# Kernel tuning notes

Hardware: AMD Instinct MI355X
Metric: run time of the kernel (lower is better)

Reference implementation:

```python
import jax, jax.numpy as jnp
import numpy as np

EMBED_DIM = 1024
NUM_HEADS = 16
HEAD_DIM = EMBED_DIM // NUM_HEADS


def setup_inputs() -> dict:
    key = jax.random.key(0)
    k1, k2, k3, k4, k5 = jax.random.split(key, 5)
    B, S, D = 2, 2048, EMBED_DIM
    s_in = 1.0 / np.sqrt(D)
    x = jax.random.normal(k1, (B, S, D), dtype=jnp.float32)
    W_qkv = jax.random.uniform(k2, (D, 3 * D), dtype=jnp.float32, minval=-s_in, maxval=s_in)
    b_qkv = jax.random.uniform(k3, (3 * D,), dtype=jnp.float32, minval=-s_in, maxval=s_in)
    W_out = jax.random.uniform(k4, (D, D), dtype=jnp.float32, minval=-s_in, maxval=s_in)
    b_out = jax.random.uniform(k5, (D,), dtype=jnp.float32, minval=-s_in, maxval=s_in)
    return {"x": x, "W_qkv": W_qkv, "b_qkv": b_qkv, "W_out": W_out, "b_out": b_out}


def reference(x, W_qkv, b_qkv, W_out, b_out):
    B, S, D = x.shape
    H, Hd = NUM_HEADS, HEAD_DIM
    qkv = x @ W_qkv + b_qkv                      # [B,S,3D]
    qkv = qkv.reshape(B, S, 3, H, Hd)
    q = qkv[:, :, 0].transpose(0, 2, 1, 3)       # [B,H,S,Hd]
    k = qkv[:, :, 1].transpose(0, 2, 1, 3)
    v = qkv[:, :, 2].transpose(0, 2, 1, 3)
    scores = jnp.einsum('bhsd,bhtd->bhst', q, k) / jnp.sqrt(jnp.float32(Hd))
    attn = jax.nn.softmax(scores, axis=-1)       # dropout is identity in eval mode
    out = jnp.einsum('bhst,bhtd->bhsd', attn, v)
    out = out.transpose(0, 2, 1, 3).reshape(B, S, D)
    return out @ W_out + b_out
```

## Files before the change

### kernel.cpp

```cpp
#include <hip/hip_runtime.h>
#include <stdint.h>
#include <math.h>

#define EMBED 1024
#define HEADS 16
#define HDIM  64
#define SEQ   2048
#define BATCH 2

typedef __bf16 bf16x8 __attribute__((ext_vector_type(8)));
typedef float  f32x4  __attribute__((ext_vector_type(4)));
typedef unsigned short u16x8 __attribute__((ext_vector_type(8)));
typedef unsigned short u16x4 __attribute__((ext_vector_type(4)));
typedef uint32_t u32x4v __attribute__((ext_vector_type(4)));

static __device__ __forceinline__ unsigned short f2bf(float f){
  union { float f; uint32_t u; } v; v.f = f;
  uint32_t u = v.u;
  uint32_t r = (u + 0x7FFFu + ((u >> 16) & 1u)) >> 16;
  return (unsigned short)r;
}
static __device__ __forceinline__ bf16x8 as_bf(u16x8 v){ return __builtin_bit_cast(bf16x8, v); }

static __device__ __forceinline__ uint32_t pk_bf16(float a, float b){
#if defined(__has_builtin) && __has_builtin(__builtin_amdgcn_cvt_pk_bf16_f32)
  typedef __bf16 bf16x2 __attribute__((ext_vector_type(2)));
  bf16x2 p = __builtin_amdgcn_cvt_pk_bf16_f32(a, b);
  return __builtin_bit_cast(uint32_t, p);
#else
  return (uint32_t)f2bf(a) | ((uint32_t)f2bf(b) << 16);
#endif
}

static __device__ __forceinline__ float fexp2(float x){
#if defined(__has_builtin) && __has_builtin(__builtin_amdgcn_exp2f)
  return __builtin_amdgcn_exp2f(x);
#else
  return exp2f(x);
#endif
}

static __device__ __forceinline__ void stage16(const unsigned short* gp,
                                               unsigned short* lp_wave, int lane){
#if defined(__has_builtin) && __has_builtin(__builtin_amdgcn_global_load_lds)
  __builtin_amdgcn_global_load_lds((const __attribute__((address_space(1))) void*)gp,
                                   (__attribute__((address_space(3))) void*)lp_wave,
                                   16, 0, 0);
#else
  *(u16x8*)(lp_wave + lane * 8) = *(const u16x8*)gp;
#endif
}

__global__ __launch_bounds__(256) void prep(
    const float* __restrict__ x,      unsigned short* __restrict__ xb,
    const float* __restrict__ W_qkv,  unsigned short* __restrict__ wqkvT,
    const float* __restrict__ W_out,  unsigned short* __restrict__ woutT)
{
  __shared__ unsigned short T[32 * 36];
  const int bid = blockIdx.x;
  const int t   = threadIdx.x;

  if (bid < 4096){
    int i = (bid * 256 + t) * 4;
    float4 v = *(const float4*)(x + i);
    u16x4 o;
    o[0] = f2bf(v.x); o[1] = f2bf(v.y); o[2] = f2bf(v.z); o[3] = f2bf(v.w);
    *(u16x4*)(xb + i) = o;
    return;
  }
  const float* W; unsigned short* Wt; int N, n0, k0;
  if (bid < 7168){
    int idx = bid - 4096;
    W = W_qkv; Wt = wqkvT; N = 3072;
    n0 = (idx % 96) * 32; k0 = (idx / 96) * 32;
  } else {
    int idx = bid - 7168;
    W = W_out; Wt = woutT; N = 1024;
    n0 = (idx & 31) * 32; k0 = (idx >> 5) * 32;
  }
  int kr = t >> 3, nc = (t & 7) * 4;
  float4 wv = *(const float4*)(W + (size_t)(k0 + kr) * N + n0 + nc);
  T[(nc + 0) * 36 + kr] = f2bf(wv.x);
  T[(nc + 1) * 36 + kr] = f2bf(wv.y);
  T[(nc + 2) * 36 + kr] = f2bf(wv.z);
  T[(nc + 3) * 36 + kr] = f2bf(wv.w);
  __syncthreads();
  int nr = t >> 3, kc = (t & 7) * 4;
  *(u16x4*)(Wt + (size_t)(n0 + nr) * 1024 + k0 + kc) = *(const u16x4*)&T[nr * 36 + kc];
}

__global__ __launch_bounds__(256) void vtrans(const unsigned short* __restrict__ V,
                                              unsigned short* __restrict__ VT){
  __shared__ unsigned short T[32 * 36];
  int t = threadIdx.x;
  int s0 = blockIdx.x * 32, d0 = blockIdx.y * 32;
  size_t base = (size_t)blockIdx.z * SEQ * HDIM;
  int sr = t >> 3, dc = (t & 7) * 4;
  u16x4 vv = *(const u16x4*)(V + base + (size_t)(s0 + sr) * HDIM + d0 + dc);
  T[(dc + 0) * 36 + sr] = vv[0];
  T[(dc + 1) * 36 + sr] = vv[1];
  T[(dc + 2) * 36 + sr] = vv[2];
  T[(dc + 3) * 36 + sr] = vv[3];
  __syncthreads();
  int dr = t >> 3, sc = (t & 7) * 4;
  int pos = (((sc >> 2) & 3) << 3) + (((sc >> 4) & 1) << 2);
  *(u16x4*)(VT + base + (size_t)(d0 + dr) * SEQ + s0 + pos) = *(const u16x4*)&T[dr * 36 + sc];
}

__global__ __launch_bounds__(256) void gemm_qkv(
    const unsigned short* __restrict__ A,
    const unsigned short* __restrict__ Bt,
    const float* __restrict__ bias,
    unsigned short* __restrict__ q_ws,
    unsigned short* __restrict__ k_ws,
    unsigned short* __restrict__ v_ws,
    int M, int N, int K)
{
  __shared__ unsigned short As[128 * 64];
  __shared__ unsigned short Bs[128 * 64];
  const int tid  = threadIdx.x;
  const int bm   = blockIdx.x, bn = blockIdx.y;
  const int w    = tid >> 6, lane = tid & 63;
  const int quad = lane >> 4, l16 = lane & 15;
  const int wm   = (w >> 1) * 64, wn = (w & 1) * 64;

  f32x4 acc[4][4] = {};

  for (int k0 = 0; k0 < K; k0 += 64) {
    #pragma unroll
    for (int i = 0; i < 4; i++){
      int c = w * 4 + i;
      int row = c * 8 + (lane >> 3);
      int kg = (lane & 7) ^ (row & 7);
      stage16(A  + (size_t)(bm * 128 + row) * K + k0 + kg * 8, &As[c * 512], lane);
      stage16(Bt + (size_t)(bn * 128 + row) * K + k0 + kg * 8, &Bs[c * 512], lane);
    }
    __syncthreads();

    #pragma unroll
    for (int kk = 0; kk < 2; kk++){
      bf16x8 af[4], bfr[4];
      #pragma unroll
      for (int t = 0; t < 4; t++){
        int ra = wm + t * 16 + l16;
        int rb = wn + t * 16 + l16;
        af[t]  = as_bf(*(const u16x8*)&As[(ra << 6) + ((((kk << 2) + quad) ^ (ra & 7)) << 3)]);
        bfr[t] = as_bf(*(const u16x8*)&Bs[(rb << 6) + ((((kk << 2) + quad) ^ (rb & 7)) << 3)]);
      }
      #pragma unroll
      for (int mt = 0; mt < 4; mt++)
        #pragma unroll
        for (int nt = 0; nt < 4; nt++)
          acc[mt][nt] = __builtin_amdgcn_mfma_f32_16x16x32_bf16(af[mt], bfr[nt], acc[mt][nt], 0, 0, 0);
    }
    __syncthreads();
  }

  const int which = (bn * 128) >> 10;
  unsigned short* dst = (which == 0) ? q_ws : (which == 1) ? k_ws : v_ws;
  const float scale = (which == 0) ? 0.18033688f : 1.0f;
  const int b = bm >> 4;
  #pragma unroll
  for (int nt = 0; nt < 4; nt++){
    int gnb = bn * 128 + wn + nt * 16;
    int h   = (gnb & 1023) >> 6;
    int hd  = (gnb & 63) + l16;
    float bv = bias[gnb + l16];
    unsigned short* dp = dst + (size_t)(b * HEADS + h) * SEQ * HDIM + hd;
    #pragma unroll
    for (int mt = 0; mt < 4; mt++){
      int s0 = ((bm & 15) * 128) + wm + mt * 16 + quad * 4;
      #pragma unroll
      for (int r = 0; r < 4; r++)
        dp[(size_t)(s0 + r) * HDIM] = f2bf((acc[mt][nt][r] + bv) * scale);
    }
  }
}

__global__ __launch_bounds__(256) void gemm_out(
    const unsigned short* __restrict__ A,
    const unsigned short* __restrict__ Bt,
    const float* __restrict__ bias,
    float* __restrict__ Cout,
    int M, int N, int K)
{
  __shared__ unsigned short As[128 * 64];
  __shared__ unsigned short Bs[64 * 64];
  const int tid  = threadIdx.x;
  const int bm   = blockIdx.x, bn = blockIdx.y;
  const int w    = tid >> 6, lane = tid & 63;
  const int quad = lane >> 4, l16 = lane & 15;
  const int wm   = (w >> 1) * 64, wn = (w & 1) * 32;

  f32x4 acc[4][2] = {};

  for (int k0 = 0; k0 < K; k0 += 64) {
    #pragma unroll
    for (int i = 0; i < 4; i++){
      int c = w * 4 + i;
      int row = c * 8 + (lane >> 3);
      int kg = (lane & 7) ^ (row & 7);
      stage16(A + (size_t)(bm * 128 + row) * K + k0 + kg * 8, &As[c * 512], lane);
    }
    #pragma unroll
    for (int i = 0; i < 2; i++){
      int c = w * 2 + i;
      int row = c * 8 + (lane >> 3);
      int kg = (lane & 7) ^ (row & 7);
      stage16(Bt + (size_t)(bn * 64 + row) * K + k0 + kg * 8, &Bs[c * 512], lane);
    }
    __syncthreads();

    #pragma unroll
    for (int kk = 0; kk < 2; kk++){
      bf16x8 af[4], bfr[2];
      #pragma unroll
      for (int t = 0; t < 4; t++){
        int ra = wm + t * 16 + l16;
        af[t] = as_bf(*(const u16x8*)&As[(ra << 6) + ((((kk << 2) + quad) ^ (ra & 7)) << 3)]);
      }
      #pragma unroll
      for (int t = 0; t < 2; t++){
        int rb = wn + t * 16 + l16;
        bfr[t] = as_bf(*(const u16x8*)&Bs[(rb << 6) + ((((kk << 2) + quad) ^ (rb & 7)) << 3)]);
      }
      #pragma unroll
      for (int mt = 0; mt < 4; mt++)
        #pragma unroll
        for (int nt = 0; nt < 2; nt++)
          acc[mt][nt] = __builtin_amdgcn_mfma_f32_16x16x32_bf16(af[mt], bfr[nt], acc[mt][nt], 0, 0, 0);
    }
    __syncthreads();
  }

  #pragma unroll
  for (int mt = 0; mt < 4; mt++)
    #pragma unroll
    for (int nt = 0; nt < 2; nt++)
      #pragma unroll
      for (int r = 0; r < 4; r++){
        int gm = bm * 128 + wm + mt * 16 + quad * 4 + r;
        int gn = bn * 64 + wn + nt * 16 + l16;
        Cout[(size_t)gm * N + gn] = acc[mt][nt][r] + bias[gn];
      }
}

__global__ __launch_bounds__(512) void attn(
    const unsigned short* __restrict__ q_ws,
    const unsigned short* __restrict__ k_ws,
    const unsigned short* __restrict__ vt_ws,
    unsigned short* __restrict__ o_ws)
{
  __shared__ unsigned short Qs[256 * 64];
  __shared__ unsigned short Ks[2][64 * 64];
  __shared__ unsigned short VTs[2][64 * 64];
  const int tid  = threadIdx.x;
  const int wgid = blockIdx.x;
  const int lin  = (wgid & 7) * 32 + (wgid >> 3);
  const int bh   = lin >> 3, qt = lin & 7;
  const int w    = tid >> 6, lane = tid & 63;
  const int quad = lane >> 4, l16 = lane & 15;
  const size_t base = (size_t)bh * SEQ * HDIM;

  #pragma unroll
  for (int i = 0; i < 4; i++){
    int c = w * 4 + i;
    int row = c * 8 + (lane >> 3);
    int kg = (lane & 7) ^ (row & 7);
    stage16(q_ws + base + (size_t)(qt * 256 + row) * HDIM + kg * 8, &Qs[c * 512], lane);
  }

  const int srow = w * 8 + (lane >> 3);
  const int skg  = (lane & 7) ^ (srow & 7);
  const int dofs = w * 512 + lane * 8;

  stage16(k_ws  + base + (size_t)srow * HDIM + skg * 8, &Ks[0][w * 512],  lane);
  stage16(vt_ws + base + (size_t)srow * SEQ + skg * 8,  &VTs[0][w * 512], lane);
  __syncthreads();

  bf16x8 bq[2][2];
  #pragma unroll
  for (int mq = 0; mq < 2; mq++){
    int row = w * 32 + mq * 16 + l16;
    #pragma unroll
    for (int ks = 0; ks < 2; ks++)
      bq[mq][ks] = as_bf(*(const u16x8*)&Qs[(row << 6) + ((((ks << 2) + quad) ^ (row & 7)) << 3)]);
  }

  const unsigned short* kp = k_ws  + base + (size_t)(64 + srow) * HDIM + skg * 8;
  const unsigned short* vp = vt_ws + base + (size_t)srow * SEQ + 64 + skg * 8;

  f32x4 acc[2][4] = {};
  float li[2] = {0.f, 0.f};

  for (int kt2 = 0; kt2 < SEQ / 128; kt2++){
    #pragma unroll
    for (int half = 0; half < 2; half++){
      const int cur = half;
      const int kt  = kt2 * 2 + half;
      u16x8 kpre, vpre;
      if (kt < SEQ / 64 - 1){
        kpre = *(const u16x8*)kp;  kp += 64 * HDIM;
        vpre = *(const u16x8*)vp;  vp += 64;
      }

      f32x4 sf[4][2] = {};
      #pragma unroll
      for (int ks = 0; ks < 2; ks++){
        #pragma unroll
        for (int nt = 0; nt < 4; nt++){
          int rk = nt * 16 + l16;
          bf16x8 ak = as_bf(*(const u16x8*)&Ks[cur][(rk << 6) + ((((ks << 2) + quad) ^ (rk & 7)) << 3)]);
          #pragma unroll
          for (int mq = 0; mq < 2; mq++)
            sf[nt][mq] = __builtin_amdgcn_mfma_f32_16x16x32_bf16(ak, bq[mq][ks], sf[nt][mq], 0, 0, 0);
        }
      }

      #pragma unroll
      for (int nt = 0; nt < 4; nt++)
        #pragma unroll
        for (int mq = 0; mq < 2; mq++)
          #pragma unroll
          for (int r = 0; r < 4; r++)
            sf[nt][mq][r] = fexp2(sf[nt][mq][r]);
      #pragma unroll
      for (int mq = 0; mq < 2; mq++)
        #pragma unroll
        for (int nt = 0; nt < 4; nt++)
          li[mq] += (sf[nt][mq][0] + sf[nt][mq][1]) + (sf[nt][mq][2] + sf[nt][mq][3]);

      #pragma unroll
      for (int c = 0; c < 2; c++){
        bf16x8 ap[2];
        #pragma unroll
        for (int mq = 0; mq < 2; mq++){
          u32x4v aw;
          aw[0] = pk_bf16(sf[c * 2][mq][0],     sf[c * 2][mq][1]);
          aw[1] = pk_bf16(sf[c * 2][mq][2],     sf[c * 2][mq][3]);
          aw[2] = pk_bf16(sf[c * 2 + 1][mq][0], sf[c * 2 + 1][mq][1]);
          aw[3] = pk_bf16(sf[c * 2 + 1][mq][2], sf[c * 2 + 1][mq][3]);
          ap[mq] = __builtin_bit_cast(bf16x8, aw);
        }
        #pragma unroll
        for (int nt = 0; nt < 4; nt++){
          int rv = nt * 16 + l16;
          bf16x8 bv = as_bf(*(const u16x8*)&VTs[cur][(rv << 6) + ((((c << 2) + quad) ^ (rv & 7)) << 3)]);
          #pragma unroll
          for (int mq = 0; mq < 2; mq++)
            acc[mq][nt] = __builtin_amdgcn_mfma_f32_16x16x32_bf16(ap[mq], bv, acc[mq][nt], 0, 0, 0);
        }
      }

      if (kt < SEQ / 64 - 1){
        *(u16x8*)&Ks[cur ^ 1][dofs]  = kpre;
        *(u16x8*)&VTs[cur ^ 1][dofs] = vpre;
      }
      __syncthreads();
    }
  }

  #pragma unroll
  for (int mq = 0; mq < 2; mq++){
    li[mq] += __shfl_xor(li[mq], 16);
    li[mq] += __shfl_xor(li[mq], 32);
  }
  float inv[2] = {1.0f / li[0], 1.0f / li[1]};
  float invr[2][4];
  #pragma unroll
  for (int mq = 0; mq < 2; mq++)
    #pragma unroll
    for (int r = 0; r < 4; r++)
      invr[mq][r] = __shfl(inv[mq], quad * 4 + r);

  int b = bh >> 4, h = bh & 15;
  #pragma unroll
  for (int mq = 0; mq < 2; mq++)
    #pragma unroll
    for (int nt = 0; nt < 4; nt++)
      #pragma unroll
      for (int r = 0; r < 4; r++){
        int s = qt * 256 + w * 32 + mq * 16 + quad * 4 + r;
        int d = h * 64 + nt * 16 + l16;
        o_ws[((size_t)(b * SEQ + s)) * EMBED + d] = f2bf(acc[mq][nt][r] * invr[mq][r]);
      }
}

extern "C" void kernel_launch(void* const* d_in, const int* in_sizes, int n_in,
                              void* d_out, int out_size, void* d_ws, size_t ws_size,
                              hipStream_t stream) {
  const float* x     = (const float*)d_in[0];
  const float* W_qkv = (const float*)d_in[1];
  const float* b_qkv = (const float*)d_in[2];
  const float* W_out = (const float*)d_in[3];
  const float* b_out = (const float*)d_in[4];
  float* out = (float*)d_out;

  char* ws = (char*)d_ws;
  unsigned short* xb    = (unsigned short*)(ws);
  unsigned short* vt    = (unsigned short*)(ws);
  unsigned short* q     = (unsigned short*)(ws + ((size_t)8  << 20));
  unsigned short* k     = (unsigned short*)(ws + ((size_t)16 << 20));
  unsigned short* v     = (unsigned short*)(ws + ((size_t)24 << 20));
  unsigned short* o     = (unsigned short*)(ws + ((size_t)24 << 20));
  unsigned short* wqkvT = (unsigned short*)(ws + ((size_t)32 << 20));
  unsigned short* woutT = (unsigned short*)(ws + ((size_t)38 << 20));

  prep<<<dim3(8192), dim3(256), 0, stream>>>(x, xb, W_qkv, wqkvT, W_out, woutT);

  gemm_qkv<<<dim3(32, 24), dim3(256), 0, stream>>>(
      xb, wqkvT, b_qkv, q, k, v, 4096, 3072, 1024);

  vtrans<<<dim3(64, 2, 32), dim3(256), 0, stream>>>(v, vt);

  attn<<<dim3(256), dim3(512), 0, stream>>>(q, k, vt, o);

  gemm_out<<<dim3(32, 16), dim3(256), 0, stream>>>(
      o, woutT, b_out, out, 4096, 1024, 1024);
}
```

Before: 197.5 us.

## Fuse V transpose into QKV GEMM epilogue and shrink attention blocks

```diff
diff --git a/kernel.cpp b/kernel.cpp
--- a/kernel.cpp
+++ b/kernel.cpp
@@ -89,31 +89,13 @@
   *(u16x4*)(Wt + (size_t)(n0 + nr) * 1024 + k0 + kc) = *(const u16x4*)&T[nr * 36 + kc];
 }
 
-__global__ __launch_bounds__(256) void vtrans(const unsigned short* __restrict__ V,
-                                              unsigned short* __restrict__ VT){
-  __shared__ unsigned short T[32 * 36];
-  int t = threadIdx.x;
-  int s0 = blockIdx.x * 32, d0 = blockIdx.y * 32;
-  size_t base = (size_t)blockIdx.z * SEQ * HDIM;
-  int sr = t >> 3, dc = (t & 7) * 4;
-  u16x4 vv = *(const u16x4*)(V + base + (size_t)(s0 + sr) * HDIM + d0 + dc);
-  T[(dc + 0) * 36 + sr] = vv[0];
-  T[(dc + 1) * 36 + sr] = vv[1];
-  T[(dc + 2) * 36 + sr] = vv[2];
-  T[(dc + 3) * 36 + sr] = vv[3];
-  __syncthreads();
-  int dr = t >> 3, sc = (t & 7) * 4;
-  int pos = (((sc >> 2) & 3) << 3) + (((sc >> 4) & 1) << 2);
-  *(u16x4*)(VT + base + (size_t)(d0 + dr) * SEQ + s0 + pos) = *(const u16x4*)&T[dr * 36 + sc];
-}
-
 __global__ __launch_bounds__(256) void gemm_qkv(
     const unsigned short* __restrict__ A,
     const unsigned short* __restrict__ Bt,
     const float* __restrict__ bias,
     unsigned short* __restrict__ q_ws,
     unsigned short* __restrict__ k_ws,
-    unsigned short* __restrict__ v_ws,
+    unsigned short* __restrict__ vt_ws,
     int M, int N, int K)
 {
   __shared__ unsigned short As[128 * 64];
@@ -157,9 +139,31 @@
   }
 
   const int which = (bn * 128) >> 10;
-  unsigned short* dst = (which == 0) ? q_ws : (which == 1) ? k_ws : v_ws;
+  const int b = bm >> 4;
+  const int S_base = (bm & 15) * 128 + wm;
+
+  if (which == 2){
+    #pragma unroll
+    for (int nt = 0; nt < 4; nt++){
+      int gnb = bn * 128 + wn + nt * 16;
+      int h   = (gnb & 1023) >> 6;
+      int d   = (gnb & 63) + l16;
+      float bv = bias[gnb + l16];
+      unsigned short* vp = vt_ws + (size_t)(b * HEADS + h) * SEQ * HDIM + (size_t)d * SEQ;
+      #pragma unroll
+      for (int mt = 0; mt < 4; mt++){
+        int spos = S_base + (mt >> 1) * 32 + quad * 8 + (mt & 1) * 4;
+        u16x4 o4;
+        #pragma unroll
+        for (int r = 0; r < 4; r++) o4[r] = f2bf(acc[mt][nt][r] + bv);
+        *(u16x4*)(vp + spos) = o4;
+      }
+    }
+    return;
+  }
+
+  unsigned short* dst = (which == 0) ? q_ws : k_ws;
   const float scale = (which == 0) ? 0.18033688f : 1.0f;
-  const int b = bm >> 4;
   #pragma unroll
   for (int nt = 0; nt < 4; nt++){
     int gnb = bn * 128 + wn + nt * 16;
@@ -169,7 +173,7 @@
     unsigned short* dp = dst + (size_t)(b * HEADS + h) * SEQ * HDIM + hd;
     #pragma unroll
     for (int mt = 0; mt < 4; mt++){
-      int s0 = ((bm & 15) * 128) + wm + mt * 16 + quad * 4;
+      int s0 = S_base + mt * 16 + quad * 4;
       #pragma unroll
       for (int r = 0; r < 4; r++)
         dp[(size_t)(s0 + r) * HDIM] = f2bf((acc[mt][nt][r] + bv) * scale);
@@ -245,145 +249,126 @@
       }
 }
 
-__global__ __launch_bounds__(512) void attn(
+__global__ __launch_bounds__(256, 4) void attn(
     const unsigned short* __restrict__ q_ws,
     const unsigned short* __restrict__ k_ws,
     const unsigned short* __restrict__ vt_ws,
     unsigned short* __restrict__ o_ws)
 {
-  __shared__ unsigned short Qs[256 * 64];
   __shared__ unsigned short Ks[2][64 * 64];
   __shared__ unsigned short VTs[2][64 * 64];
   const int tid  = threadIdx.x;
   const int wgid = blockIdx.x;
-  const int lin  = (wgid & 7) * 32 + (wgid >> 3);
-  const int bh   = lin >> 3, qt = lin & 7;
+  const int lin  = (wgid & 7) * 128 + (wgid >> 3);
+  const int bh   = lin >> 5, qt = lin & 31;
   const int w    = tid >> 6, lane = tid & 63;
   const int quad = lane >> 4, l16 = lane & 15;
   const size_t base = (size_t)bh * SEQ * HDIM;
 
-  #pragma unroll
-  for (int i = 0; i < 4; i++){
-    int c = w * 4 + i;
-    int row = c * 8 + (lane >> 3);
-    int kg = (lane & 7) ^ (row & 7);
-    stage16(q_ws + base + (size_t)(qt * 256 + row) * HDIM + kg * 8, &Qs[c * 512], lane);
-  }
-
-  const int srow = w * 8 + (lane >> 3);
-  const int skg  = (lane & 7) ^ (srow & 7);
-  const int dofs = w * 512 + lane * 8;
-
-  stage16(k_ws  + base + (size_t)srow * HDIM + skg * 8, &Ks[0][w * 512],  lane);
-  stage16(vt_ws + base + (size_t)srow * SEQ + skg * 8,  &VTs[0][w * 512], lane);
+  bf16x8 bq[2];
+  {
+    const int qrow = qt * 64 + w * 16 + l16;
+    #pragma unroll
+    for (int ks = 0; ks < 2; ks++)
+      bq[ks] = as_bf(*(const u16x8*)(q_ws + base + (size_t)qrow * HDIM + (ks * 4 + quad) * 8));
+  }
+
+  const int row0  = w * 16 + (lane >> 3);
+  const int row1  = row0 + 8;
+  const int kg0   = (lane & 7) ^ (row0 & 7);
+  const int kg1   = (lane & 7) ^ (row1 & 7);
+  const int dofs0 = (w * 2 + 0) * 512 + lane * 8;
+  const int dofs1 = (w * 2 + 1) * 512 + lane * 8;
+
+  stage16(k_ws  + base + (size_t)row0 * HDIM + kg0 * 8, &Ks[0][(w * 2 + 0) * 512], lane);
+  stage16(k_ws  + base + (size_t)row1 * HDIM + kg1 * 8, &Ks[0][(w * 2 + 1) * 512], lane);
+  stage16(vt_ws + base + (size_t)row0 * SEQ + kg0 * 8,  &VTs[0][(w * 2 + 0) * 512], lane);
+  stage16(vt_ws + base + (size_t)row1 * SEQ + kg1 * 8,  &VTs[0][(w * 2 + 1) * 512], lane);
   __syncthreads();
 
-  bf16x8 bq[2][2];
-  #pragma unroll
-  for (int mq = 0; mq < 2; mq++){
-    int row = w * 32 + mq * 16 + l16;
-    #pragma unroll
-    for (int ks = 0; ks < 2; ks++)
-      bq[mq][ks] = as_bf(*(const u16x8*)&Qs[(row << 6) + ((((ks << 2) + quad) ^ (row & 7)) << 3)]);
-  }
-
-  const unsigned short* kp = k_ws  + base + (size_t)(64 + srow) * HDIM + skg * 8;
-  const unsigned short* vp = vt_ws + base + (size_t)srow * SEQ + 64 + skg * 8;
-
-  f32x4 acc[2][4] = {};
-  float li[2] = {0.f, 0.f};
+  const unsigned short* kp0 = k_ws  + base + (size_t)(64 + row0) * HDIM + kg0 * 8;
+  const unsigned short* kp1 = k_ws  + base + (size_t)(64 + row1) * HDIM + kg1 * 8;
+  const unsigned short* vp0 = vt_ws + base + (size_t)row0 * SEQ + 64 + kg0 * 8;
+  const unsigned short* vp1 = vt_ws + base + (size_t)row1 * SEQ + 64 + kg1 * 8;
+
+  f32x4 acc[4] = {};
+  float li = 0.f;
 
   for (int kt2 = 0; kt2 < SEQ / 128; kt2++){
     #pragma unroll
     for (int half = 0; half < 2; half++){
       const int cur = half;
       const int kt  = kt2 * 2 + half;
-      u16x8 kpre, vpre;
+      u16x8 kpre0, kpre1, vpre0, vpre1;
       if (kt < SEQ / 64 - 1){
-        kpre = *(const u16x8*)kp;  kp += 64 * HDIM;
-        vpre = *(const u16x8*)vp;  vp += 64;
-      }
-
-      f32x4 sf[4][2] = {};
-      #pragma unroll
-      for (int ks = 0; ks < 2; ks++){
+        kpre0 = *(const u16x8*)kp0;  kp0 += 64 * HDIM;
+        kpre1 = *(const u16x8*)kp1;  kp1 += 64 * HDIM;
+        vpre0 = *(const u16x8*)vp0;  vp0 += 64;
+        vpre1 = *(const u16x8*)vp1;  vp1 += 64;
+      }
+
+      f32x4 sf[4] = {};
+      #pragma unroll
+      for (int ks = 0; ks < 2; ks++)
         #pragma unroll
         for (int nt = 0; nt < 4; nt++){
           int rk = nt * 16 + l16;
           bf16x8 ak = as_bf(*(const u16x8*)&Ks[cur][(rk << 6) + ((((ks << 2) + quad) ^ (rk & 7)) << 3)]);
-          #pragma unroll
-          for (int mq = 0; mq < 2; mq++)
-            sf[nt][mq] = __builtin_amdgcn_mfma_f32_16x16x32_bf16(ak, bq[mq][ks], sf[nt][mq], 0, 0, 0);
+          sf[nt] = __builtin_amdgcn_mfma_f32_16x16x32_bf16(ak, bq[ks], sf[nt], 0, 0, 0);
         }
-      }
 
       #pragma unroll
       for (int nt = 0; nt < 4; nt++)
         #pragma unroll
-        for (int mq = 0; mq < 2; mq++)
-          #pragma unroll
-          for (int r = 0; r < 4; r++)
-            sf[nt][mq][r] = fexp2(sf[nt][mq][r]);
-      #pragma unroll
-      for (int mq = 0; mq < 2; mq++)
-        #pragma unroll
-        for (int nt = 0; nt < 4; nt++)
-          li[mq] += (sf[nt][mq][0] + sf[nt][mq][1]) + (sf[nt][mq][2] + sf[nt][mq][3]);
+        for (int r = 0; r < 4; r++)
+          sf[nt][r] = fexp2(sf[nt][r]);
+      #pragma unroll
+      for (int nt = 0; nt < 4; nt++)
+        li += (sf[nt][0] + sf[nt][1]) + (sf[nt][2] + sf[nt][3]);
 
       #pragma unroll
       for (int c = 0; c < 2; c++){
-        bf16x8 ap[2];
-        #pragma unroll
-        for (int mq = 0; mq < 2; mq++){
-          u32x4v aw;
-          aw[0] = pk_bf16(sf[c * 2][mq][0],     sf[c * 2][mq][1]);
-          aw[1] = pk_bf16(sf[c * 2][mq][2],     sf[c * 2][mq][3]);
-          aw[2] = pk_bf16(sf[c * 2 + 1][mq][0], sf[c * 2 + 1][mq][1]);
-          aw[3] = pk_bf16(sf[c * 2 + 1][mq][2], sf[c * 2 + 1][mq][3]);
-          ap[mq] = __builtin_bit_cast(bf16x8, aw);
-        }
+        u32x4v aw;
+        aw[0] = pk_bf16(sf[c * 2][0],     sf[c * 2][1]);
+        aw[1] = pk_bf16(sf[c * 2][2],     sf[c * 2][3]);
+        aw[2] = pk_bf16(sf[c * 2 + 1][0], sf[c * 2 + 1][1]);
+        aw[3] = pk_bf16(sf[c * 2 + 1][2], sf[c * 2 + 1][3]);
+        bf16x8 ap = __builtin_bit_cast(bf16x8, aw);
         #pragma unroll
         for (int nt = 0; nt < 4; nt++){
           int rv = nt * 16 + l16;
           bf16x8 bv = as_bf(*(const u16x8*)&VTs[cur][(rv << 6) + ((((c << 2) + quad) ^ (rv & 7)) << 3)]);
-          #pragma unroll
-          for (int mq = 0; mq < 2; mq++)
-            acc[mq][nt] = __builtin_amdgcn_mfma_f32_16x16x32_bf16(ap[mq], bv, acc[mq][nt], 0, 0, 0);
+          acc[nt] = __builtin_amdgcn_mfma_f32_16x16x32_bf16(ap, bv, acc[nt], 0, 0, 0);
         }
       }
 
       if (kt < SEQ / 64 - 1){
-        *(u16x8*)&Ks[cur ^ 1][dofs]  = kpre;
-        *(u16x8*)&VTs[cur ^ 1][dofs] = vpre;
+        *(u16x8*)&Ks[cur ^ 1][dofs0]  = kpre0;
+        *(u16x8*)&Ks[cur ^ 1][dofs1]  = kpre1;
+        *(u16x8*)&VTs[cur ^ 1][dofs0] = vpre0;
+        *(u16x8*)&VTs[cur ^ 1][dofs1] = vpre1;
       }
       __syncthreads();
     }
   }
 
+  li += __shfl_xor(li, 16);
+  li += __shfl_xor(li, 32);
+  float inv = 1.0f / li;
+  float invr[4];
   #pragma unroll
-  for (int mq = 0; mq < 2; mq++){
-    li[mq] += __shfl_xor(li[mq], 16);
-    li[mq] += __shfl_xor(li[mq], 32);
-  }
-  float inv[2] = {1.0f / li[0], 1.0f / li[1]};
-  float invr[2][4];
-  #pragma unroll
-  for (int mq = 0; mq < 2; mq++)
-    #pragma unroll
-    for (int r = 0; r < 4; r++)
-      invr[mq][r] = __shfl(inv[mq], quad * 4 + r);
+  for (int r = 0; r < 4; r++)
+    invr[r] = __shfl(inv, quad * 4 + r);
 
   int b = bh >> 4, h = bh & 15;
   #pragma unroll
-  for (int mq = 0; mq < 2; mq++)
-    #pragma unroll
-    for (int nt = 0; nt < 4; nt++)
-      #pragma unroll
-      for (int r = 0; r < 4; r++){
-        int s = qt * 256 + w * 32 + mq * 16 + quad * 4 + r;
-        int d = h * 64 + nt * 16 + l16;
-        o_ws[((size_t)(b * SEQ + s)) * EMBED + d] = f2bf(acc[mq][nt][r] * invr[mq][r]);
-      }
+  for (int nt = 0; nt < 4; nt++)
+    #pragma unroll
+    for (int r = 0; r < 4; r++){
+      int s = qt * 64 + w * 16 + quad * 4 + r;
+      int d = h * 64 + nt * 16 + l16;
+      o_ws[((size_t)(b * SEQ + s)) * EMBED + d] = f2bf(acc[nt][r] * invr[r]);
+    }
 }
 
 extern "C" void kernel_launch(void* const* d_in, const int* in_sizes, int n_in,
@@ -398,22 +383,19 @@
 
   char* ws = (char*)d_ws;
   unsigned short* xb    = (unsigned short*)(ws);
-  unsigned short* vt    = (unsigned short*)(ws);
+  unsigned short* o     = (unsigned short*)(ws);
   unsigned short* q     = (unsigned short*)(ws + ((size_t)8  << 20));
   unsigned short* k     = (unsigned short*)(ws + ((size_t)16 << 20));
-  unsigned short* v     = (unsigned short*)(ws + ((size_t)24 << 20));
-  unsigned short* o     = (unsigned short*)(ws + ((size_t)24 << 20));
+  unsigned short* vt    = (unsigned short*)(ws + ((size_t)24 << 20));
   unsigned short* wqkvT = (unsigned short*)(ws + ((size_t)32 << 20));
   unsigned short* woutT = (unsigned short*)(ws + ((size_t)38 << 20));
 
   prep<<<dim3(8192), dim3(256), 0, stream>>>(x, xb, W_qkv, wqkvT, W_out, woutT);
 
   gemm_qkv<<<dim3(32, 24), dim3(256), 0, stream>>>(
-      xb, wqkvT, b_qkv, q, k, v, 4096, 3072, 1024);
-
-  vtrans<<<dim3(64, 2, 32), dim3(256), 0, stream>>>(v, vt);
-
-  attn<<<dim3(256), dim3(512), 0, stream>>>(q, k, vt, o);
+      xb, wqkvT, b_qkv, q, k, vt, 4096, 3072, 1024);
+
+  attn<<<dim3(1024), dim3(256), 0, stream>>>(q, k, vt, o);
 
   gemm_out<<<dim3(32, 16), dim3(256), 0, stream>>>(
       o, woutT, b_out, out, 4096, 1024, 1024);
```

Result: faster. 191.9 us (-2.8%).

## Split pipeline by batch and co-schedule attention with GEMMs in combo kernels

Applied to the files above, without the earlier changes.

```diff
diff --git a/kernel.cpp b/kernel.cpp
--- a/kernel.cpp
+++ b/kernel.cpp
@@ -89,37 +89,19 @@
   *(u16x4*)(Wt + (size_t)(n0 + nr) * 1024 + k0 + kc) = *(const u16x4*)&T[nr * 36 + kc];
 }
 
-__global__ __launch_bounds__(256) void vtrans(const unsigned short* __restrict__ V,
-                                              unsigned short* __restrict__ VT){
-  __shared__ unsigned short T[32 * 36];
-  int t = threadIdx.x;
-  int s0 = blockIdx.x * 32, d0 = blockIdx.y * 32;
-  size_t base = (size_t)blockIdx.z * SEQ * HDIM;
-  int sr = t >> 3, dc = (t & 7) * 4;
-  u16x4 vv = *(const u16x4*)(V + base + (size_t)(s0 + sr) * HDIM + d0 + dc);
-  T[(dc + 0) * 36 + sr] = vv[0];
-  T[(dc + 1) * 36 + sr] = vv[1];
-  T[(dc + 2) * 36 + sr] = vv[2];
-  T[(dc + 3) * 36 + sr] = vv[3];
-  __syncthreads();
-  int dr = t >> 3, sc = (t & 7) * 4;
-  int pos = (((sc >> 2) & 3) << 3) + (((sc >> 4) & 1) << 2);
-  *(u16x4*)(VT + base + (size_t)(d0 + dr) * SEQ + s0 + pos) = *(const u16x4*)&T[dr * 36 + sc];
-}
-
-__global__ __launch_bounds__(256) void gemm_qkv(
+static __device__ __forceinline__ void gemm_qkv_body(
+    int bm, int bn, unsigned short* SM,
     const unsigned short* __restrict__ A,
     const unsigned short* __restrict__ Bt,
     const float* __restrict__ bias,
     unsigned short* __restrict__ q_ws,
     unsigned short* __restrict__ k_ws,
-    unsigned short* __restrict__ v_ws,
-    int M, int N, int K)
-{
-  __shared__ unsigned short As[128 * 64];
-  __shared__ unsigned short Bs[128 * 64];
+    unsigned short* __restrict__ vt_ws)
+{
+  unsigned short* As = SM;
+  unsigned short* Bs = SM + 8192;
+  const int K = 1024;
   const int tid  = threadIdx.x;
-  const int bm   = blockIdx.x, bn = blockIdx.y;
   const int w    = tid >> 6, lane = tid & 63;
   const int quad = lane >> 4, l16 = lane & 15;
   const int wm   = (w >> 1) * 64, wn = (w & 1) * 64;
@@ -132,8 +114,8 @@
       int c = w * 4 + i;
       int row = c * 8 + (lane >> 3);
       int kg = (lane & 7) ^ (row & 7);
-      stage16(A  + (size_t)(bm * 128 + row) * K + k0 + kg * 8, &As[c * 512], lane);
-      stage16(Bt + (size_t)(bn * 128 + row) * K + k0 + kg * 8, &Bs[c * 512], lane);
+      stage16(A  + (size_t)(bm * 128 + row) * K + k0 + kg * 8, As + c * 512, lane);
+      stage16(Bt + (size_t)(bn * 128 + row) * K + k0 + kg * 8, Bs + c * 512, lane);
     }
     __syncthreads();
 
@@ -157,9 +139,31 @@
   }
 
   const int which = (bn * 128) >> 10;
-  unsigned short* dst = (which == 0) ? q_ws : (which == 1) ? k_ws : v_ws;
+  const int b = bm >> 4;
+  const int S_base = (bm & 15) * 128 + wm;
+
+  if (which == 2){
+    #pragma unroll
+    for (int nt = 0; nt < 4; nt++){
+      int gnb = bn * 128 + wn + nt * 16;
+      int h   = (gnb & 1023) >> 6;
+      int d   = (gnb & 63) + l16;
+      float bv = bias[gnb + l16];
+      unsigned short* vp = vt_ws + (size_t)(b * HEADS + h) * SEQ * HDIM + (size_t)d * SEQ;
+      #pragma unroll
+      for (int mt = 0; mt < 4; mt++){
+        int spos = S_base + (mt >> 1) * 32 + quad * 8 + (mt & 1) * 4;
+        u16x4 o4;
+        #pragma unroll
+        for (int r = 0; r < 4; r++) o4[r] = f2bf(acc[mt][nt][r] + bv);
+        *(u16x4*)(vp + spos) = o4;
+      }
+    }
+    return;
+  }
+
+  unsigned short* dst = (which == 0) ? q_ws : k_ws;
   const float scale = (which == 0) ? 0.18033688f : 1.0f;
-  const int b = bm >> 4;
   #pragma unroll
   for (int nt = 0; nt < 4; nt++){
     int gnb = bn * 128 + wn + nt * 16;
@@ -169,7 +173,7 @@
     unsigned short* dp = dst + (size_t)(b * HEADS + h) * SEQ * HDIM + hd;
     #pragma unroll
     for (int mt = 0; mt < 4; mt++){
-      int s0 = ((bm & 15) * 128) + wm + mt * 16 + quad * 4;
+      int s0 = S_base + mt * 16 + quad * 4;
       #pragma unroll
       for (int r = 0; r < 4; r++)
         dp[(size_t)(s0 + r) * HDIM] = f2bf((acc[mt][nt][r] + bv) * scale);
@@ -177,17 +181,17 @@
   }
 }
 
-__global__ __launch_bounds__(256) void gemm_out(
+static __device__ __forceinline__ void gemm_out_body(
+    int bm, int bn, unsigned short* SM,
     const unsigned short* __restrict__ A,
     const unsigned short* __restrict__ Bt,
     const float* __restrict__ bias,
-    float* __restrict__ Cout,
-    int M, int N, int K)
-{
-  __shared__ unsigned short As[128 * 64];
-  __shared__ unsigned short Bs[64 * 64];
+    float* __restrict__ Cout)
+{
+  unsigned short* As = SM;
+  unsigned short* Bs = SM + 8192;
+  const int K = 1024, N = 1024;
   const int tid  = threadIdx.x;
-  const int bm   = blockIdx.x, bn = blockIdx.y;
   const int w    = tid >> 6, lane = tid & 63;
   const int quad = lane >> 4, l16 = lane & 15;
   const int wm   = (w >> 1) * 64, wn = (w & 1) * 32;
@@ -200,14 +204,14 @@
       int c = w * 4 + i;
       int row = c * 8 + (lane >> 3);
       int kg = (lane & 7) ^ (row & 7);
-      stage16(A + (size_t)(bm * 128 + row) * K + k0 + kg * 8, &As[c * 512], lane);
+      stage16(A + (size_t)(bm * 128 + row) * K + k0 + kg * 8, As + c * 512, lane);
     }
     #pragma unroll
     for (int i = 0; i < 2; i++){
       int c = w * 2 + i;
       int row = c * 8 + (lane >> 3);
       int kg = (lane & 7) ^ (row & 7);
-      stage16(Bt + (size_t)(bn * 64 + row) * K + k0 + kg * 8, &Bs[c * 512], lane);
+      stage16(Bt + (size_t)(bn * 64 + row) * K + k0 + kg * 8, Bs + c * 512, lane);
     }
     __syncthreads();
 
@@ -245,119 +249,114 @@
       }
 }
 
-__global__ __launch_bounds__(512) void attn(
+static __device__ __forceinline__ void attn_body(
+    int abid, int bh_base, unsigned short* SM,
     const unsigned short* __restrict__ q_ws,
     const unsigned short* __restrict__ k_ws,
     const unsigned short* __restrict__ vt_ws,
     unsigned short* __restrict__ o_ws)
 {
-  __shared__ unsigned short Qs[256 * 64];
-  __shared__ unsigned short Ks[2][64 * 64];
-  __shared__ unsigned short VTs[2][64 * 64];
+  unsigned short* Ks  = SM;
+  unsigned short* VTs = SM + 8192;
   const int tid  = threadIdx.x;
-  const int wgid = blockIdx.x;
-  const int lin  = (wgid & 7) * 32 + (wgid >> 3);
-  const int bh   = lin >> 3, qt = lin & 7;
+  const int bh   = bh_base + (abid >> 4);
+  const int qt   = abid & 15;
   const int w    = tid >> 6, lane = tid & 63;
   const int quad = lane >> 4, l16 = lane & 15;
   const size_t base = (size_t)bh * SEQ * HDIM;
 
-  #pragma unroll
-  for (int i = 0; i < 4; i++){
-    int c = w * 4 + i;
-    int row = c * 8 + (lane >> 3);
-    int kg = (lane & 7) ^ (row & 7);
-    stage16(q_ws + base + (size_t)(qt * 256 + row) * HDIM + kg * 8, &Qs[c * 512], lane);
-  }
-
-  const int srow = w * 8 + (lane >> 3);
-  const int skg  = (lane & 7) ^ (srow & 7);
-  const int dofs = w * 512 + lane * 8;
-
-  stage16(k_ws  + base + (size_t)srow * HDIM + skg * 8, &Ks[0][w * 512],  lane);
-  stage16(vt_ws + base + (size_t)srow * SEQ + skg * 8,  &VTs[0][w * 512], lane);
+  bf16x8 bq[2][2];
+  #pragma unroll
+  for (int mq = 0; mq < 2; mq++){
+    int qrow = qt * 128 + w * 32 + mq * 16 + l16;
+    #pragma unroll
+    for (int ks = 0; ks < 2; ks++)
+      bq[mq][ks] = as_bf(*(const u16x8*)(q_ws + base + (size_t)qrow * HDIM + (ks * 4 + quad) * 8));
+  }
+
+  const int row0 = w * 16 + (lane >> 3), row1 = row0 + 8;
+  const int kg0 = (lane & 7) ^ (row0 & 7), kg1 = (lane & 7) ^ (row1 & 7);
+  const int dofs0 = (w * 2) * 512 + lane * 8, dofs1 = dofs0 + 512;
+
+  stage16(k_ws  + base + (size_t)row0 * HDIM + kg0 * 8, Ks  + (w * 2) * 512,     lane);
+  stage16(k_ws  + base + (size_t)row1 * HDIM + kg1 * 8, Ks  + (w * 2 + 1) * 512, lane);
+  stage16(vt_ws + base + (size_t)row0 * SEQ + kg0 * 8,  VTs + (w * 2) * 512,     lane);
+  stage16(vt_ws + base + (size_t)row1 * SEQ + kg1 * 8,  VTs + (w * 2 + 1) * 512, lane);
   __syncthreads();
 
-  bf16x8 bq[2][2];
-  #pragma unroll
-  for (int mq = 0; mq < 2; mq++){
-    int row = w * 32 + mq * 16 + l16;
-    #pragma unroll
-    for (int ks = 0; ks < 2; ks++)
-      bq[mq][ks] = as_bf(*(const u16x8*)&Qs[(row << 6) + ((((ks << 2) + quad) ^ (row & 7)) << 3)]);
-  }
-
-  const unsigned short* kp = k_ws  + base + (size_t)(64 + srow) * HDIM + skg * 8;
-  const unsigned short* vp = vt_ws + base + (size_t)srow * SEQ + 64 + skg * 8;
+  const unsigned short* kp0 = k_ws  + base + (size_t)(64 + row0) * HDIM + kg0 * 8;
+  const unsigned short* kp1 = k_ws  + base + (size_t)(64 + row1) * HDIM + kg1 * 8;
+  const unsigned short* vp0 = vt_ws + base + (size_t)row0 * SEQ + 64 + kg0 * 8;
+  const unsigned short* vp1 = vt_ws + base + (size_t)row1 * SEQ + 64 + kg1 * 8;
 
   f32x4 acc[2][4] = {};
   float li[2] = {0.f, 0.f};
 
-  for (int kt2 = 0; kt2 < SEQ / 128; kt2++){
-    #pragma unroll
-    for (int half = 0; half < 2; half++){
-      const int cur = half;
-      const int kt  = kt2 * 2 + half;
-      u16x8 kpre, vpre;
-      if (kt < SEQ / 64 - 1){
-        kpre = *(const u16x8*)kp;  kp += 64 * HDIM;
-        vpre = *(const u16x8*)vp;  vp += 64;
-      }
-
-      f32x4 sf[4][2] = {};
-      #pragma unroll
-      for (int ks = 0; ks < 2; ks++){
-        #pragma unroll
-        for (int nt = 0; nt < 4; nt++){
-          int rk = nt * 16 + l16;
-          bf16x8 ak = as_bf(*(const u16x8*)&Ks[cur][(rk << 6) + ((((ks << 2) + quad) ^ (rk & 7)) << 3)]);
-          #pragma unroll
-          for (int mq = 0; mq < 2; mq++)
-            sf[nt][mq] = __builtin_amdgcn_mfma_f32_16x16x32_bf16(ak, bq[mq][ks], sf[nt][mq], 0, 0, 0);
-        }
-      }
-
+  for (int kt = 0; kt < SEQ / 64; kt++){
+    const int co = (kt & 1) * 4096;
+    u16x8 kpre0, kpre1, vpre0, vpre1;
+    if (kt < SEQ / 64 - 1){
+      kpre0 = *(const u16x8*)kp0;  kp0 += 64 * HDIM;
+      kpre1 = *(const u16x8*)kp1;  kp1 += 64 * HDIM;
+      vpre0 = *(const u16x8*)vp0;  vp0 += 64;
+      vpre1 = *(const u16x8*)vp1;  vp1 += 64;
+    }
+
+    f32x4 sf[4][2] = {};
+    #pragma unroll
+    for (int ks = 0; ks < 2; ks++)
+      #pragma unroll
+      for (int nt = 0; nt < 4; nt++){
+        int rk = nt * 16 + l16;
+        bf16x8 ak = as_bf(*(const u16x8*)&Ks[co + (rk << 6) + ((((ks << 2) + quad) ^ (rk & 7)) << 3)]);
+        #pragma unroll
+        for (int mq = 0; mq < 2; mq++)
+          sf[nt][mq] = __builtin_amdgcn_mfma_f32_16x16x32_bf16(ak, bq[mq][ks], sf[nt][mq], 0, 0, 0);
+      }
+
+    #pragma unroll
+    for (int nt = 0; nt < 4; nt++)
+      #pragma unroll
+      for (int mq = 0; mq < 2; mq++)
+        #pragma unroll
+        for (int r = 0; r < 4; r++)
+          sf[nt][mq][r] = fexp2(sf[nt][mq][r]);
+    #pragma unroll
+    for (int mq = 0; mq < 2; mq++)
       #pragma unroll
       for (int nt = 0; nt < 4; nt++)
+        li[mq] += (sf[nt][mq][0] + sf[nt][mq][1]) + (sf[nt][mq][2] + sf[nt][mq][3]);
+
+    #pragma unroll
+    for (int c = 0; c < 2; c++){
+      bf16x8 ap[2];
+      #pragma unroll
+      for (int mq = 0; mq < 2; mq++){
+        u32x4v aw;
+        aw[0] = pk_bf16(sf[c * 2][mq][0],     sf[c * 2][mq][1]);
+        aw[1] = pk_bf16(sf[c * 2][mq][2],     sf[c * 2][mq][3]);
+        aw[2] = pk_bf16(sf[c * 2 + 1][mq][0], sf[c * 2 + 1][mq][1]);
+        aw[3] = pk_bf16(sf[c * 2 + 1][mq][2], sf[c * 2 + 1][mq][3]);
+        ap[mq] = __builtin_bit_cast(bf16x8, aw);
+      }
+      #pragma unroll
+      for (int nt = 0; nt < 4; nt++){
+        int rv = nt * 16 + l16;
+        bf16x8 bv = as_bf(*(const u16x8*)&VTs[co + (rv << 6) + ((((c << 2) + quad) ^ (rv & 7)) << 3)]);
         #pragma unroll
         for (int mq = 0; mq < 2; mq++)
-          #pragma unroll
-          for (int r = 0; r < 4; r++)
-            sf[nt][mq][r] = fexp2(sf[nt][mq][r]);
-      #pragma unroll
-      for (int mq = 0; mq < 2; mq++)
-        #pragma unroll
-        for (int nt = 0; nt < 4; nt++)
-          li[mq] += (sf[nt][mq][0] + sf[nt][mq][1]) + (sf[nt][mq][2] + sf[nt][mq][3]);
-
-      #pragma unroll
-      for (int c = 0; c < 2; c++){
-        bf16x8 ap[2];
-        #pragma unroll
-        for (int mq = 0; mq < 2; mq++){
-          u32x4v aw;
-          aw[0] = pk_bf16(sf[c * 2][mq][0],     sf[c * 2][mq][1]);
-          aw[1] = pk_bf16(sf[c * 2][mq][2],     sf[c * 2][mq][3]);
-          aw[2] = pk_bf16(sf[c * 2 + 1][mq][0], sf[c * 2 + 1][mq][1]);
-          aw[3] = pk_bf16(sf[c * 2 + 1][mq][2], sf[c * 2 + 1][mq][3]);
-          ap[mq] = __builtin_bit_cast(bf16x8, aw);
-        }
-        #pragma unroll
-        for (int nt = 0; nt < 4; nt++){
-          int rv = nt * 16 + l16;
-          bf16x8 bv = as_bf(*(const u16x8*)&VTs[cur][(rv << 6) + ((((c << 2) + quad) ^ (rv & 7)) << 3)]);
-          #pragma unroll
-          for (int mq = 0; mq < 2; mq++)
-            acc[mq][nt] = __builtin_amdgcn_mfma_f32_16x16x32_bf16(ap[mq], bv, acc[mq][nt], 0, 0, 0);
-        }
-      }
-
-      if (kt < SEQ / 64 - 1){
-        *(u16x8*)&Ks[cur ^ 1][dofs]  = kpre;
-        *(u16x8*)&VTs[cur ^ 1][dofs] = vpre;
-      }
-      __syncthreads();
-    }
+          acc[mq][nt] = __builtin_amdgcn_mfma_f32_16x16x32_bf16(ap[mq], bv, acc[mq][nt], 0, 0, 0);
+      }
+    }
+
+    if (kt < SEQ / 64 - 1){
+      const int no = (co ^ 4096);
+      *(u16x8*)&Ks[no + dofs0]  = kpre0;
+      *(u16x8*)&Ks[no + dofs1]  = kpre1;
+      *(u16x8*)&VTs[no + dofs0] = vpre0;
+      *(u16x8*)&VTs[no + dofs1] = vpre1;
+    }
+    __syncthreads();
   }
 
   #pragma unroll
@@ -380,10 +379,56 @@
     for (int nt = 0; nt < 4; nt++)
       #pragma unroll
       for (int r = 0; r < 4; r++){
-        int s = qt * 256 + w * 32 + mq * 16 + quad * 4 + r;
+        int s = qt * 128 + w * 32 + mq * 16 + quad * 4 + r;
         int d = h * 64 + nt * 16 + l16;
         o_ws[((size_t)(b * SEQ + s)) * EMBED + d] = f2bf(acc[mq][nt][r] * invr[mq][r]);
       }
+}
+
+__global__ __launch_bounds__(256) void qkv_part(
+    const unsigned short* __restrict__ A, const unsigned short* __restrict__ Bt,
+    const float* __restrict__ bias,
+    unsigned short* q, unsigned short* k, unsigned short* vt, int bm_base)
+{
+  __shared__ unsigned short SM[16384];
+  gemm_qkv_body(bm_base + (blockIdx.x & 15), blockIdx.x >> 4, SM, A, Bt, bias, q, k, vt);
+}
+
+__global__ __launch_bounds__(256) void out_part(
+    const unsigned short* __restrict__ A, const unsigned short* __restrict__ Bt,
+    const float* __restrict__ bias, float* C, int bm_base)
+{
+  __shared__ unsigned short SM[16384];
+  gemm_out_body(bm_base + (blockIdx.x & 15), blockIdx.x >> 4, SM, A, Bt, bias, C);
+}
+
+__global__ __launch_bounds__(256) void combo_attn0_qkv1(
+    const unsigned short* __restrict__ xb, const unsigned short* __restrict__ wqkvT,
+    const float* __restrict__ b_qkv,
+    unsigned short* q, unsigned short* k, unsigned short* vt, unsigned short* o)
+{
+  __shared__ unsigned short SM[16384];
+  if (blockIdx.x < 256)
+    attn_body(blockIdx.x, 0, SM, q, k, vt, o);
+  else {
+    int g = blockIdx.x - 256;
+    gemm_qkv_body(16 + (g & 15), g >> 4, SM, xb, wqkvT, b_qkv, q, k, vt);
+  }
+}
+
+__global__ __launch_bounds__(256) void combo_attn1_out0(
+    const unsigned short* __restrict__ q, const unsigned short* __restrict__ k,
+    const unsigned short* __restrict__ vt, unsigned short* o,
+    const unsigned short* __restrict__ woutT, const float* __restrict__ b_out,
+    float* out)
+{
+  __shared__ unsigned short SM[16384];
+  if (blockIdx.x < 256)
+    attn_body(blockIdx.x, 16, SM, q, k, vt, o);
+  else {
+    int g = blockIdx.x - 256;
+    gemm_out_body(g & 15, g >> 4, SM, o, woutT, b_out, out);
+  }
 }
 
 extern "C" void kernel_launch(void* const* d_in, const int* in_sizes, int n_in,
@@ -398,23 +443,20 @@
 
   char* ws = (char*)d_ws;
   unsigned short* xb    = (unsigned short*)(ws);
-  unsigned short* vt    = (unsigned short*)(ws);
+  unsigned short* o     = (unsigned short*)(ws);
   unsigned short* q     = (unsigned short*)(ws + ((size_t)8  << 20));
   unsigned short* k     = (unsigned short*)(ws + ((size_t)16 << 20));
-  unsigned short* v     = (unsigned short*)(ws + ((size_t)24 << 20));
-  unsigned short* o     = (unsigned short*)(ws + ((size_t)24 << 20));
+  unsigned short* vt    = (unsigned short*)(ws + ((size_t)24 << 20));
   unsigned short* wqkvT = (unsigned short*)(ws + ((size_t)32 << 20));
   unsigned short* woutT = (unsigned short*)(ws + ((size_t)38 << 20));
 
   prep<<<dim3(8192), dim3(256), 0, stream>>>(x, xb, W_qkv, wqkvT, W_out, woutT);
 
-  gemm_qkv<<<dim3(32, 24), dim3(256), 0, stream>>>(
-      xb, wqkvT, b_qkv, q, k, v, 4096, 3072, 1024);
-
-  vtrans<<<dim3(64, 2, 32), dim3(256), 0, stream>>>(v, vt);
-
-  attn<<<dim3(256), dim3(512), 0, stream>>>(q, k, vt, o);
-
-  gemm_out<<<dim3(32, 16), dim3(256), 0, stream>>>(
-      o, woutT, b_out, out, 4096, 1024, 1024);
-}
+  qkv_part<<<dim3(384), dim3(256), 0, stream>>>(xb, wqkvT, b_qkv, q, k, vt, 0);
+
+  combo_attn0_qkv1<<<dim3(640), dim3(256), 0, stream>>>(xb, wqkvT, b_qkv, q, k, vt, o);
+
+  combo_attn1_out0<<<dim3(512), dim3(256), 0, stream>>>(q, k, vt, o, woutT, b_out, out);
+
+  out_part<<<dim3(256), dim3(256), 0, stream>>>(o, woutT, b_out, out, 16);
+}
```

After: 210.8 us. +6.7%, slower.
